# Kernel tuning notes

Measured on AMD Instinct MI355X. Metric: run time of the kernel, lower is better.

Reference implementation:

```python
import jax, jax.numpy as jnp
import numpy as np

N = 4096
CIN = 128
COUT = 128
J = 2
SLOPE = 0.2        # LeakyReLU negative slope (GAT-style)
NEG = -9.0e15      # mask fill value from the source
ATT = J * COUT     # att_slice


def _leaky(v):
    return jnp.where(v >= 0, v, SLOPE * v)


def setup_inputs() -> dict:
    key = jax.random.key(0)
    ks = jax.random.split(key, 12)
    x = jax.random.normal(ks[0], (N, CIN), dtype=jnp.float32)

    def sparse_op(k):
        kv, km = jax.random.split(k)
        vals = jax.random.normal(kv, (N, N), dtype=jnp.float32)
        mask = jax.random.uniform(km, (N, N)) < 0.05
        return jnp.where(mask, vals, 0.0)

    Lu = sparse_op(ks[1])
    Ld = sparse_op(ks[2])
    P = jax.random.normal(ks[3], (N, N), dtype=jnp.float32) * 0.01  # harmonic projector

    s = 1.0 / np.sqrt(CIN)
    Wi_w = jax.random.uniform(ks[4], (J, CIN, COUT), minval=-s, maxval=s)
    Wi_b = jax.random.uniform(ks[5], (J, COUT), minval=-s, maxval=s)
    Ws_w = jax.random.uniform(ks[6], (J, CIN, COUT), minval=-s, maxval=s)
    Ws_b = jax.random.uniform(ks[7], (J, COUT), minval=-s, maxval=s)
    Wh_w = jax.random.uniform(ks[8], (CIN, COUT), minval=-s, maxval=s)
    Wh_b = jax.random.uniform(ks[9], (COUT,), minval=-s, maxval=s)
    att_irr = jax.random.normal(ks[10], (2 * ATT, 1), dtype=jnp.float32) * 0.1
    att_sol = jax.random.normal(ks[11], (2 * ATT, 1), dtype=jnp.float32) * 0.1
    return {"x": x, "Lu": Lu, "Ld": Ld, "P": P,
            "Wi_w": Wi_w, "Wi_b": Wi_b, "Ws_w": Ws_w, "Ws_b": Ws_b,
            "Wh_w": Wh_w, "Wh_b": Wh_b, "att_irr": att_irr, "att_sol": att_sol}


def reference(x, Lu, Ld, P, Wi_w, Wi_b, Ws_w, Ws_b, Wh_w, Wh_b, att_irr, att_sol):
    n = x.shape[0]
    # concat_j W_irr[j](x) -> [N, J*COUT] (j-major matches torch.cat along dim=1)
    x_irr = (jnp.einsum('nc,jco->njo', x, Wi_w) + Wi_b[None]).reshape(n, ATT)
    x_sol = (jnp.einsum('nc,jco->njo', x, Ws_w) + Ws_b[None]).reshape(n, ATT)

    # GAT-style scores: E[i,j] = leaky(s1[i] + s2[j])
    E_irr = _leaky(x_irr @ att_irr[:ATT] + (x_irr @ att_irr[ATT:]).T)
    E_sol = _leaky(x_sol @ att_sol[:ATT] + (x_sol @ att_sol[ATT:]).T)
    E_irr = jnp.where(Ld != 0, E_irr, NEG)
    E_sol = jnp.where(Lu != 0, E_sol, NEG)
    alpha_irr = jax.nn.softmax(E_irr, axis=1)  # dropout: eval mode -> identity
    alpha_sol = jax.nn.softmax(E_sol, axis=1)

    z = (alpha_irr @ x) @ Wi_w[0] + Wi_b[0] + (alpha_sol @ x) @ Ws_w[0] + Ws_b[0]
    for p in range(1, J):  # Laplacian-power aggregation
        alpha_irr = alpha_irr @ Ld
        alpha_sol = alpha_sol @ Lu
        z = z + (alpha_irr @ x) @ Wi_w[p] + Wi_b[p]
        z = z + (alpha_sol @ x) @ Ws_w[p] + Ws_b[p]
    z = z + (P @ x) @ Wh_w + Wh_b
    return z
```

## Files before the change

kernel.cpp:

```cpp
#include <hip/hip_runtime.h>

#define NN 4096
#define IDX_CAP 512
#define SEG_CAP 160
#define SLOPE 0.2f

typedef float f4_t __attribute__((ext_vector_type(4)));
typedef __bf16 bf8v __attribute__((ext_vector_type(8)));
typedef float f32x16 __attribute__((ext_vector_type(16)));

#define V_OFF     0
#define C_OFF     512
#define BT_OFF    516
#define S_OFF     1024
#define HXI_OFF   32768
#define HXS_OFF   (HXI_OFF + NN*128)
#define UI_OFF    (HXS_OFF + NN*128)
#define US_OFF    (UI_OFF + NN*128)
#define XWH_OFF   (US_OFF + NN*128)
#define OI_OFF    (XWH_OFF + NN*128)
#define OS_OFF    (OI_OFF + NN*128)
#define ZP_OFF    (OS_OFF + NN*128)
#define WS_FLOATS (ZP_OFF + 8*NN*128)
#define IDX_BYTE_OFF ((size_t)WS_FLOATS * 4)
#define CNT_BYTE_OFF (IDX_BYTE_OFF + (size_t)2*NN*IDX_CAP*2)

#define XI(c)   ((c) + (((c) >> 5) << 2))

#define MAP_BR(bid)   (((bid) >> 2) & 1)
#define MAP_ROW(bid)  ((((bid) >> 3) << 2) | ((bid) & 3))

#define FRAG(c, k) ((size_t)((k) >> 4) * 2048 + (size_t)((c) >> 5) * 512 \
                    + (size_t)((((c) & 31) + 32 * (((k) >> 3) & 1)) * 8 + ((k) & 7)))

__device__ __forceinline__ unsigned short f2bf(float x) {
  unsigned u = __float_as_uint(x);
  return (unsigned short)((u + 0x7FFFu + ((u >> 16) & 1u)) >> 16);
}
__device__ __forceinline__ float bf2f(unsigned short h) {
  return __uint_as_float(((unsigned)h) << 16);
}
union BFU { unsigned short u[8]; bf8v v; };

__global__ __launch_bounds__(128) void k_prep(
    const float* __restrict__ Wi_w, const float* __restrict__ Wi_b,
    const float* __restrict__ Ws_w, const float* __restrict__ Ws_b,
    const float* __restrict__ Wh_b, const float* __restrict__ att_irr,
    const float* __restrict__ att_sol, float* __restrict__ ws) {
  const int t = threadIdx.x;
  float v1i = 0.f, v2i = 0.f, v1s = 0.f, v2s = 0.f;
  for (int j = 0; j < 2; ++j) {
    for (int o = 0; o < 128; ++o) {
      const float wi = Wi_w[j*16384 + t*128 + o];
      const float wv = Ws_w[j*16384 + t*128 + o];
      v1i += wi * att_irr[j*128 + o];
      v2i += wi * att_irr[256 + j*128 + o];
      v1s += wv * att_sol[j*128 + o];
      v2s += wv * att_sol[256 + j*128 + o];
    }
  }
  ws[V_OFF + t]       = v1i;
  ws[V_OFF + 128 + t] = v2i;
  ws[V_OFF + 256 + t] = v1s;
  ws[V_OFF + 384 + t] = v2s;
  ws[BT_OFF + t] = Wi_b[t] + Wi_b[128 + t] + Ws_b[t] + Ws_b[128 + t] + Wh_b[t];
  if (t < 4) {
    const float* bb = (t < 2) ? Wi_b : Ws_b;
    const float* aa = ((t < 2) ? att_irr : att_sol) + ((t & 1) ? 256 : 0);
    float c = 0.f;
    for (int k = 0; k < 256; ++k) c += bb[k] * aa[k];
    ws[C_OFF + t] = c;
  }
}

__global__ __launch_bounds__(256) void k_pre2(
    const float* __restrict__ x, const float* __restrict__ Wh_w,
    float* __restrict__ ws, unsigned short* __restrict__ xth,
    unsigned short* __restrict__ xtl) {
  __shared__ __align__(16) float At[32][33];
  __shared__ __align__(16) float Wt[32][144];
  const int t = threadIdx.x;

  if (blockIdx.x < 128) {
    const int rb = blockIdx.x;
    const int rg = t >> 4, cg = t & 15;
    const int r0 = rb * 32;
    float acc[2][8];
    #pragma unroll
    for (int i = 0; i < 2; ++i)
      #pragma unroll
      for (int j = 0; j < 8; ++j) acc[i][j] = 0.f;
    for (int k0 = 0; k0 < 128; k0 += 32) {
      __syncthreads();
      {
        const int row = t >> 3, kq = t & 7;
        const float4 av = *(const float4*)&x[(r0 + row)*128 + k0 + kq*4];
        At[row][kq*4+0] = av.x; At[row][kq*4+1] = av.y;
        At[row][kq*4+2] = av.z; At[row][kq*4+3] = av.w;
      }
      #pragma unroll
      for (int l = 0; l < 4; ++l) {
        const int idx = t + l*256;
        const int kr = idx >> 5, c4 = idx & 31;
        const float4 wv = *(const float4*)&Wh_w[(k0 + kr)*128 + c4*4];
        *(float4*)&Wt[kr][XI(c4*4)] = wv;
      }
      __syncthreads();
      #pragma unroll
      for (int k = 0; k < 32; ++k) {
        const float a0 = At[rg*2 + 0][k];
        const float a1 = At[rg*2 + 1][k];
        const float4 b0 = *(const float4*)&Wt[k][XI(cg*8)];
        const float4 b1 = *(const float4*)&Wt[k][XI(cg*8 + 4)];
        acc[0][0] += a0*b0.x; acc[0][1] += a0*b0.y; acc[0][2] += a0*b0.z; acc[0][3] += a0*b0.w;
        acc[0][4] += a0*b1.x; acc[0][5] += a0*b1.y; acc[0][6] += a0*b1.z; acc[0][7] += a0*b1.w;
        acc[1][0] += a1*b0.x; acc[1][1] += a1*b0.y; acc[1][2] += a1*b0.z; acc[1][3] += a1*b0.w;
        acc[1][4] += a1*b1.x; acc[1][5] += a1*b1.y; acc[1][6] += a1*b1.z; acc[1][7] += a1*b1.w;
      }
    }
    #pragma unroll
    for (int i = 0; i < 2; ++i) {
      const int r = r0 + rg*2 + i;
      #pragma unroll
      for (int j = 0; j < 8; ++j) {
        const int c = cg*8 + j;
        const float val = acc[i][j];
        const unsigned short h = f2bf(val);
        const unsigned short l = f2bf(val - bf2f(h));
        const size_t fa = FRAG(c, r);
        xth[fa] = h;
        xtl[fa] = l;
      }
    }
  } else {
    const int wave = t >> 6, lane = t & 63;
    const int row = (blockIdx.x - 128) * 4 + wave;
    const float* v = ws + V_OFF;
    const float x0 = x[row*128 + lane];
    const float x1 = x[row*128 + 64 + lane];
    float p0 = x0 * v[lane]       + x1 * v[64 + lane];
    float p1 = x0 * v[128 + lane] + x1 * v[192 + lane];
    float p2 = x0 * v[256 + lane] + x1 * v[320 + lane];
    float p3 = x0 * v[384 + lane] + x1 * v[448 + lane];
    #pragma unroll
    for (int off = 32; off; off >>= 1) {
      p0 += __shfl_down(p0, off);
      p1 += __shfl_down(p1, off);
      p2 += __shfl_down(p2, off);
      p3 += __shfl_down(p3, off);
    }
    if (lane == 0) {
      ws[S_OFF + row]          = p0 + ws[C_OFF + 0];
      ws[S_OFF + NN + row]     = p1 + ws[C_OFF + 1];
      ws[S_OFF + 2*NN + row]   = p2 + ws[C_OFF + 2];
      ws[S_OFF + 3*NN + row]   = p3 + ws[C_OFF + 3];
    }
  }
}

__global__ __launch_bounds__(256) void k_spmm_emit(
    const float* __restrict__ Ld, const float* __restrict__ Lu,
    const float* __restrict__ x, float* __restrict__ ws,
    unsigned short* __restrict__ idxbuf, int* __restrict__ cntbuf) {
  const int bid = blockIdx.x;
  const int br  = MAP_BR(bid);
  const int row = MAP_ROW(bid);
  const float* __restrict__ Lrow = (br ? Lu : Ld) + (size_t)row * NN;
  float* __restrict__ Hx = ws + (br ? HXS_OFF : HXI_OFF);
  unsigned short* __restrict__ idxg = idxbuf + (size_t)(br*NN + row) * IDX_CAP;
  const int t = threadIdx.x;
  const int w = t >> 6, lane = t & 63;
  const unsigned long long lmask = (1ull << lane) - 1ull;

  __shared__ short jseg[4][SEG_CAP];
  __shared__ float vseg[4][SEG_CAP];
  __shared__ int   wcnt[4];
  __shared__ int   off[5];
  __shared__ short jl[IDX_CAP];
  __shared__ float vl[IDX_CAP];
  __shared__ float red[4][128];

  const f4_t* __restrict__ Lrow4 = (const f4_t*)Lrow;
  f4_t lv[4];
  #pragma unroll
  for (int i = 0; i < 4; ++i) lv[i] = __builtin_nontemporal_load(&Lrow4[i*256 + t]);

  int base = 0;
  #pragma unroll
  for (int i = 0; i < 4; ++i) {
    #pragma unroll
    for (int c = 0; c < 4; ++c) {
      const float v = lv[i][c];
      const unsigned long long bm = __ballot(v != 0.f);
      if (v != 0.f) {
        const int pos = base + (int)__popcll(bm & lmask);
        if (pos < SEG_CAP) {
          jseg[w][pos] = (short)((i*256 + t)*4 + c);
          vseg[w][pos] = v;
        }
      }
      base += (int)__popcll(bm);
    }
  }
  if (lane == 0) wcnt[w] = base;
  __syncthreads();
  if (t == 0) {
    int o = 0, ov = 0;
    #pragma unroll
    for (int s = 0; s < 4; ++s) { off[s] = o; ov |= (wcnt[s] > SEG_CAP); o += wcnt[s]; }
    off[4] = (ov || o > IDX_CAP) ? (IDX_CAP + 1) : o;
    cntbuf[br*NN + row] = off[4];
  }
  __syncthreads();
  const int m = off[4];

  if (m <= IDX_CAP) {
    const int o = off[w], c = wcnt[w];
    for (int k = lane; k < c; k += 64) {
      const short j = jseg[w][k];
      jl[o + k] = j;
      vl[o + k] = vseg[w][k];
      idxg[o + k] = (unsigned short)j;
    }
  }
  __syncthreads();

  if (m <= IDX_CAP) {
    const f4_t* __restrict__ x4 = (const f4_t*)x;
    const int li = lane & 31, half = lane >> 5;
    f4_t acc = {0.f, 0.f, 0.f, 0.f};
    int p = w;
    for (; 2*(p + 12) + 1 < m; p += 16) {
      const int q0 = 2*p + half, q1 = 2*(p+4) + half,
                q2 = 2*(p+8) + half, q3 = 2*(p+12) + half;
      const int j0 = jl[q0], j1 = jl[q1], j2 = jl[q2], j3 = jl[q3];
      const float v0 = vl[q0], v1 = vl[q1], v2 = vl[q2], v3 = vl[q3];
      const f4_t g0 = x4[j0*32 + li];
      const f4_t g1 = x4[j1*32 + li];
      const f4_t g2 = x4[j2*32 + li];
      const f4_t g3 = x4[j3*32 + li];
      acc += v0*g0; acc += v1*g1; acc += v2*g2; acc += v3*g3;
    }
    for (; 2*p < m; p += 4) {
      const int q = 2*p + half;
      if (q < m) acc += vl[q] * x4[jl[q]*32 + li];
    }
    #pragma unroll
    for (int c = 0; c < 4; ++c) acc[c] += __shfl_xor(acc[c], 32);
    if (half == 0) {
      red[w][li*4+0] = acc[0]; red[w][li*4+1] = acc[1];
      red[w][li*4+2] = acc[2]; red[w][li*4+3] = acc[3];
    }
  } else {
    const float2* __restrict__ x2 = (const float2*)x;
    float acc0 = 0.f, acc1 = 0.f;
    for (int j = w*1024; j < (w+1)*1024; ++j) {
      const float v = Lrow[j];
      if (v != 0.f) {
        const float2 g = x2[j*64 + lane];
        acc0 += v*g.x; acc1 += v*g.y;
      }
    }
    red[w][lane*2]     = acc0;
    red[w][lane*2 + 1] = acc1;
  }
  __syncthreads();
  if (t < 128)
    Hx[row*128 + t] = red[0][t] + red[1][t] + red[2][t] + red[3][t];
}

__global__ __launch_bounds__(256) void k_ugemm(
    const float* __restrict__ x, const float* __restrict__ Wi_w,
    const float* __restrict__ Ws_w, float* __restrict__ ws) {
  const int rb = blockIdx.x;
  const int sel = blockIdx.y;
  const float* A[2]; const float* W[2]; float* out;
  if (sel == 0) { A[0]=x; W[0]=Wi_w; A[1]=ws+HXI_OFF; W[1]=Wi_w+16384; out=ws+UI_OFF; }
  else          { A[0]=x; W[0]=Ws_w; A[1]=ws+HXS_OFF; W[1]=Ws_w+16384; out=ws+US_OFF; }

  __shared__ __align__(16) float At[32][33];
  __shared__ __align__(16) float Wt[32][144];
  const int t = threadIdx.x;
  const int rg = t >> 4, cg = t & 15;
  const int r0 = rb * 32;
  float acc[2][8];
  #pragma unroll
  for (int i = 0; i < 2; ++i)
    #pragma unroll
    for (int j = 0; j < 8; ++j) acc[i][j] = 0.f;

  for (int ps = 0; ps < 2; ++ps) {
    const float* __restrict__ Ap = A[ps];
    const float* __restrict__ Wp = W[ps];
    for (int k0 = 0; k0 < 128; k0 += 32) {
      __syncthreads();
      {
        const int row = t >> 3, kq = t & 7;
        const float4 av = *(const float4*)&Ap[(r0 + row)*128 + k0 + kq*4];
        At[row][kq*4+0] = av.x; At[row][kq*4+1] = av.y;
        At[row][kq*4+2] = av.z; At[row][kq*4+3] = av.w;
      }
      #pragma unroll
      for (int l = 0; l < 4; ++l) {
        const int idx = t + l*256;
        const int kr = idx >> 5, c4 = idx & 31;
        const float4 wv = *(const float4*)&Wp[(k0 + kr)*128 + c4*4];
        *(float4*)&Wt[kr][XI(c4*4)] = wv;
      }
      __syncthreads();
      #pragma unroll
      for (int k = 0; k < 32; ++k) {
        const float a0 = At[rg*2 + 0][k];
        const float a1 = At[rg*2 + 1][k];
        const float4 b0 = *(const float4*)&Wt[k][XI(cg*8)];
        const float4 b1 = *(const float4*)&Wt[k][XI(cg*8 + 4)];
        acc[0][0] += a0*b0.x; acc[0][1] += a0*b0.y; acc[0][2] += a0*b0.z; acc[0][3] += a0*b0.w;
        acc[0][4] += a0*b1.x; acc[0][5] += a0*b1.y; acc[0][6] += a0*b1.z; acc[0][7] += a0*b1.w;
        acc[1][0] += a1*b0.x; acc[1][1] += a1*b0.y; acc[1][2] += a1*b0.z; acc[1][3] += a1*b0.w;
        acc[1][4] += a1*b1.x; acc[1][5] += a1*b1.y; acc[1][6] += a1*b1.z; acc[1][7] += a1*b1.w;
      }
    }
  }
  #pragma unroll
  for (int i = 0; i < 2; ++i) {
    const int r = r0 + rg*2 + i;
    #pragma unroll
    for (int j = 0; j < 8; ++j) out[r*128 + cg*8 + j] = acc[i][j];
  }
}

__global__ __launch_bounds__(256) void k_attn(
    const float* __restrict__ Ld, const float* __restrict__ Lu,
    float* __restrict__ ws, const unsigned short* __restrict__ idxbuf,
    const int* __restrict__ cntbuf) {
  const int bid = blockIdx.x;
  const int br  = MAP_BR(bid);
  const int row = MAP_ROW(bid);
  const float* __restrict__ U = ws + (br ? US_OFF : UI_OFF);
  float* __restrict__ O = ws + (br ? OS_OFF : OI_OFF);
  const float s1 = ws[S_OFF + (br ? 2*NN : 0) + row];
  const float* __restrict__ s2a = ws + S_OFF + (br ? 3*NN : NN);
  const int cnt = cntbuf[br*NN + row];
  const int t = threadIdx.x;
  const int w = t >> 6, lane = t & 63;

  __shared__ int   jl[IDX_CAP];
  __shared__ float el[IDX_CAP];
  __shared__ float red[4][128];
  __shared__ float rsum[256];
  __shared__ float dsh[4];

  if (cnt > 0 && cnt <= IDX_CAP) {
    const unsigned short* __restrict__ idx = idxbuf + (size_t)(br*NN + row) * IDX_CAP;
    float dpart = 0.f;
    for (int p = t; p < cnt; p += 256) {
      const int j = idx[p];
      const float sc = s1 + s2a[j];
      const float e = expf(sc >= 0.f ? sc : SLOPE * sc);
      jl[p] = j; el[p] = e; dpart += e;
    }
    rsum[t] = dpart;
    __syncthreads();
    if (t < 128) rsum[t] += rsum[t + 128];
    __syncthreads();
    if (t < 64) {
      float v = rsum[t] + rsum[t + 64];
      #pragma unroll
      for (int off = 32; off; off >>= 1) v += __shfl_down(v, off);
      if (t == 0) dsh[0] = v;
    }
    __syncthreads();
    const float den = dsh[0];
    const f4_t* __restrict__ U4 = (const f4_t*)U;
    const int li = lane & 31, half = lane >> 5;
    f4_t acc = {0.f, 0.f, 0.f, 0.f};
    int p = w;
    for (; 2*(p + 12) + 1 < cnt; p += 16) {
      const int q0 = 2*p + half, q1 = 2*(p+4) + half,
                q2 = 2*(p+8) + half, q3 = 2*(p+12) + half;
      const int j0 = jl[q0], j1 = jl[q1], j2 = jl[q2], j3 = jl[q3];
      const float e0 = el[q0], e1 = el[q1], e2 = el[q2], e3 = el[q3];
      const f4_t g0 = U4[j0*32 + li];
      const f4_t g1 = U4[j1*32 + li];
      const f4_t g2 = U4[j2*32 + li];
      const f4_t g3 = U4[j3*32 + li];
      acc += e0*g0; acc += e1*g1; acc += e2*g2; acc += e3*g3;
    }
    for (; 2*p < cnt; p += 4) {
      const int q = 2*p + half;
      if (q < cnt) acc += el[q] * U4[jl[q]*32 + li];
    }
    #pragma unroll
    for (int c = 0; c < 4; ++c) acc[c] += __shfl_xor(acc[c], 32);
    if (half == 0) {
      red[w][li*4+0] = acc[0]; red[w][li*4+1] = acc[1];
      red[w][li*4+2] = acc[2]; red[w][li*4+3] = acc[3];
    }
    __syncthreads();
    if (t < 128)
      O[row*128 + t] = (red[0][t] + red[1][t] + red[2][t] + red[3][t]) / den;
  } else if (cnt == 0) {
    const float2* __restrict__ U2 = (const float2*)U;
    float acc0 = 0.f, acc1 = 0.f;
    for (int j = w*1024; j < (w+1)*1024; ++j) {
      const float2 g = U2[j*64 + lane];
      acc0 += g.x; acc1 += g.y;
    }
    red[w][lane*2]     = acc0;
    red[w][lane*2 + 1] = acc1;
    __syncthreads();
    if (t < 128)
      O[row*128 + t] = (red[0][t] + red[1][t] + red[2][t] + red[3][t]) * (1.f / NN);
  } else {
    const float* __restrict__ Lrow = (br ? Lu : Ld) + (size_t)row * NN;
    const float2* __restrict__ U2 = (const float2*)U;
    float acc0 = 0.f, acc1 = 0.f, dp = 0.f;
    for (int j = w*1024; j < (w+1)*1024; ++j) {
      const float v = Lrow[j];
      if (v != 0.f) {
        const float sc = s1 + s2a[j];
        const float e = expf(sc >= 0.f ? sc : SLOPE * sc);
        const float2 g = U2[j*64 + lane];
        acc0 += e*g.x; acc1 += e*g.y;
        dp += e;
      }
    }
    if (lane == 0) dsh[w] = dp;
    red[w][lane*2]     = acc0;
    red[w][lane*2 + 1] = acc1;
    __syncthreads();
    const float den = dsh[0] + dsh[1] + dsh[2] + dsh[3];
    if (t < 128)
      O[row*128 + t] = (red[0][t] + red[1][t] + red[2][t] + red[3][t]) / den;
  }
}

__global__ __launch_bounds__(256) void k_pgemm(
    const float* __restrict__ P, const unsigned short* __restrict__ xth,
    const unsigned short* __restrict__ xtl, float* __restrict__ zpart) {
  const int t = threadIdx.x;
  const int w = t >> 6, lane = t & 63;
  const int la = lane & 31;
  const int koff = (lane >> 5) * 8;
  const int r0 = blockIdx.x * 32;
  const int kz = blockIdx.y;
  const int kb = kz * 512 + w * 128;

  f32x16 acc[4];
  #pragma unroll
  for (int n = 0; n < 4; ++n)
    #pragma unroll
    for (int e = 0; e < 16; ++e) acc[n][e] = 0.f;

  const float* __restrict__ arow = P + (size_t)(r0 + la) * NN + kb + koff;
  const unsigned short* __restrict__ bh_base = xth + (size_t)kb * 128 + lane * 8;
  const unsigned short* __restrict__ bl_base = xtl + (size_t)kb * 128 + lane * 8;

  f4_t a0 = __builtin_nontemporal_load((const f4_t*)arow);
  f4_t a1 = __builtin_nontemporal_load((const f4_t*)(arow + 4));
  for (int s = 0; s < 8; ++s) {
    f4_t na0 = a0, na1 = a1;
    if (s < 7) {
      na0 = __builtin_nontemporal_load((const f4_t*)(arow + (s + 1) * 16));
      na1 = __builtin_nontemporal_load((const f4_t*)(arow + (s + 1) * 16 + 4));
    }
    BFU ah, al;
    #pragma unroll
    for (int i = 0; i < 8; ++i) {
      const float f = (i < 4) ? a0[i] : a1[i - 4];
      const unsigned short h = f2bf(f);
      ah.u[i] = h;
      al.u[i] = f2bf(f - bf2f(h));
    }
    const unsigned short* __restrict__ bh_s = bh_base + s * 2048;
    const unsigned short* __restrict__ bl_s = bl_base + s * 2048;
    #pragma unroll
    for (int n = 0; n < 4; ++n) {
      const bf8v bh = *(const bf8v*)(bh_s + n * 512);
      const bf8v bl = *(const bf8v*)(bl_s + n * 512);
      acc[n] = __builtin_amdgcn_mfma_f32_32x32x16_bf16(ah.v, bh, acc[n], 0, 0, 0);
      acc[n] = __builtin_amdgcn_mfma_f32_32x32x16_bf16(al.v, bh, acc[n], 0, 0, 0);
      acc[n] = __builtin_amdgcn_mfma_f32_32x32x16_bf16(ah.v, bl, acc[n], 0, 0, 0);
    }
    a0 = na0; a1 = na1;
  }

  __shared__ float red[2][32][128];
  if (w < 2) {
    #pragma unroll
    for (int n = 0; n < 4; ++n)
      #pragma unroll
      for (int reg = 0; reg < 16; ++reg) {
        const int row = (reg & 3) + 8*(reg >> 2) + 4*(lane >> 5);
        red[w][row][32*n + la] = acc[n][reg];
      }
  }
  __syncthreads();
  if (w >= 2) {
    #pragma unroll
    for (int n = 0; n < 4; ++n)
      #pragma unroll
      for (int reg = 0; reg < 16; ++reg) {
        const int row = (reg & 3) + 8*(reg >> 2) + 4*(lane >> 5);
        red[w - 2][row][32*n + la] += acc[n][reg];
      }
  }
  __syncthreads();
  float* __restrict__ zp = zpart + (size_t)kz * NN * 128;
  #pragma unroll
  for (int i = 0; i < 8; ++i) {
    const int row = w * 8 + i;
    zp[(size_t)(r0 + row) * 128 + lane]      = red[0][row][lane]      + red[1][row][lane];
    zp[(size_t)(r0 + row) * 128 + 64 + lane] = red[0][row][64 + lane] + red[1][row][64 + lane];
  }
}

__global__ __launch_bounds__(256) void k_combine(const float* __restrict__ ws,
                                                 float* __restrict__ z) {
  const int i = blockIdx.x * 256 + threadIdx.x;
  const int col = i & 127;
  float acc = ws[BT_OFF + col] + ws[OI_OFF + i] + ws[OS_OFF + i];
  #pragma unroll
  for (int kz = 0; kz < 8; ++kz) acc += ws[ZP_OFF + kz*NN*128 + i];
  z[i] = acc;
}

extern "C" void kernel_launch(void* const* d_in, const int* in_sizes, int n_in,
                              void* d_out, int out_size, void* d_ws, size_t ws_size,
                              hipStream_t stream) {
  const float* x       = (const float*)d_in[0];
  const float* Lu      = (const float*)d_in[1];
  const float* Ld      = (const float*)d_in[2];
  const float* P       = (const float*)d_in[3];
  const float* Wi_w    = (const float*)d_in[4];
  const float* Wi_b    = (const float*)d_in[5];
  const float* Ws_w    = (const float*)d_in[6];
  const float* Ws_b    = (const float*)d_in[7];
  const float* Wh_w    = (const float*)d_in[8];
  const float* Wh_b    = (const float*)d_in[9];
  const float* att_irr = (const float*)d_in[10];
  const float* att_sol = (const float*)d_in[11];
  float* z  = (float*)d_out;
  float* ws = (float*)d_ws;
  unsigned short* idxbuf = (unsigned short*)((char*)d_ws + IDX_BYTE_OFF);
  int*            cntbuf = (int*)((char*)d_ws + CNT_BYTE_OFF);
  float*          zpart  = ws + ZP_OFF;
  unsigned short* xth    = (unsigned short*)(ws + XWH_OFF);
  unsigned short* xtl    = xth + (size_t)128 * NN;

  k_prep<<<1, 128, 0, stream>>>(Wi_w, Wi_b, Ws_w, Ws_b, Wh_b, att_irr, att_sol, ws);
  k_pre2<<<1152, 256, 0, stream>>>(x, Wh_w, ws, xth, xtl);
  k_spmm_emit<<<2 * NN, 256, 0, stream>>>(Ld, Lu, x, ws, idxbuf, cntbuf);
  {
    dim3 g(128, 2);
    k_ugemm<<<g, 256, 0, stream>>>(x, Wi_w, Ws_w, ws);
  }
  k_attn<<<2 * NN, 256, 0, stream>>>(Ld, Lu, ws, idxbuf, cntbuf);
  {
    dim3 g(128, 8);
    k_pgemm<<<g, 256, 0, stream>>>(P, xth, xtl, zpart);
  }
  k_combine<<<NN * 128 / 256, 256, 0, stream>>>(ws, z);
}
```

Measured before the change: 353.8 us.

## Map one row per wavefront in sparse emit and attention kernels

```diff
diff --git a/kernel.cpp b/kernel.cpp
--- a/kernel.cpp
+++ b/kernel.cpp
@@ -2,7 +2,6 @@
 
 #define NN 4096
 #define IDX_CAP 512
-#define SEG_CAP 160
 #define SLOPE 0.2f
 
 typedef float f4_t __attribute__((ext_vector_type(4)));
@@ -27,8 +26,8 @@
 
 #define XI(c)   ((c) + (((c) >> 5) << 2))
 
-#define MAP_BR(bid)   (((bid) >> 2) & 1)
-#define MAP_ROW(bid)  ((((bid) >> 3) << 2) | ((bid) & 3))
+#define BMAP_BR(bid)    (((bid) >> 2) & 1)
+#define BMAP_RBLK(bid)  ((((bid) >> 3) << 2) | ((bid) & 3))
 
 #define FRAG(c, k) ((size_t)((k) >> 4) * 2048 + (size_t)((c) >> 5) * 512 \
                     + (size_t)((((c) & 31) + 32 * (((k) >> 3) & 1)) * 8 + ((k) & 7)))
@@ -163,110 +162,85 @@
     const float* __restrict__ x, float* __restrict__ ws,
     unsigned short* __restrict__ idxbuf, int* __restrict__ cntbuf) {
   const int bid = blockIdx.x;
-  const int br  = MAP_BR(bid);
-  const int row = MAP_ROW(bid);
+  const int br  = BMAP_BR(bid);
+  const int w = threadIdx.x >> 6, lane = threadIdx.x & 63;
+  const int row = BMAP_RBLK(bid) * 4 + w;
   const float* __restrict__ Lrow = (br ? Lu : Ld) + (size_t)row * NN;
   float* __restrict__ Hx = ws + (br ? HXS_OFF : HXI_OFF);
   unsigned short* __restrict__ idxg = idxbuf + (size_t)(br*NN + row) * IDX_CAP;
-  const int t = threadIdx.x;
-  const int w = t >> 6, lane = t & 63;
   const unsigned long long lmask = (1ull << lane) - 1ull;
 
-  __shared__ short jseg[4][SEG_CAP];
-  __shared__ float vseg[4][SEG_CAP];
-  __shared__ int   wcnt[4];
-  __shared__ int   off[5];
-  __shared__ short jl[IDX_CAP];
-  __shared__ float vl[IDX_CAP];
-  __shared__ float red[4][128];
+  __shared__ short jl[4][IDX_CAP];
+  __shared__ float vl[4][IDX_CAP];
 
   const f4_t* __restrict__ Lrow4 = (const f4_t*)Lrow;
-  f4_t lv[4];
-  #pragma unroll
-  for (int i = 0; i < 4; ++i) lv[i] = __builtin_nontemporal_load(&Lrow4[i*256 + t]);
-
   int base = 0;
   #pragma unroll
-  for (int i = 0; i < 4; ++i) {
-    #pragma unroll
-    for (int c = 0; c < 4; ++c) {
-      const float v = lv[i][c];
-      const unsigned long long bm = __ballot(v != 0.f);
-      if (v != 0.f) {
-        const int pos = base + (int)__popcll(bm & lmask);
-        if (pos < SEG_CAP) {
-          jseg[w][pos] = (short)((i*256 + t)*4 + c);
-          vseg[w][pos] = v;
+  for (int c = 0; c < 4; ++c) {
+    f4_t lv[4];
+    #pragma unroll
+    for (int i = 0; i < 4; ++i)
+      lv[i] = __builtin_nontemporal_load(&Lrow4[c*256 + i*64 + lane]);
+    #pragma unroll
+    for (int i = 0; i < 4; ++i) {
+      #pragma unroll
+      for (int cc = 0; cc < 4; ++cc) {
+        const float v = lv[i][cc];
+        const unsigned long long bm = __ballot(v != 0.f);
+        if (v != 0.f) {
+          const int pos = base + (int)__popcll(bm & lmask);
+          if (pos < IDX_CAP) {
+            jl[w][pos] = (short)((c*256 + i*64 + lane)*4 + cc);
+            vl[w][pos] = v;
+          }
         }
-      }
-      base += (int)__popcll(bm);
-    }
-  }
-  if (lane == 0) wcnt[w] = base;
-  __syncthreads();
-  if (t == 0) {
-    int o = 0, ov = 0;
-    #pragma unroll
-    for (int s = 0; s < 4; ++s) { off[s] = o; ov |= (wcnt[s] > SEG_CAP); o += wcnt[s]; }
-    off[4] = (ov || o > IDX_CAP) ? (IDX_CAP + 1) : o;
-    cntbuf[br*NN + row] = off[4];
-  }
-  __syncthreads();
-  const int m = off[4];
+        base += (int)__popcll(bm);
+      }
+    }
+  }
+  const int m = base;
+  if (lane == 0) cntbuf[br*NN + row] = m;
 
   if (m <= IDX_CAP) {
-    const int o = off[w], c = wcnt[w];
-    for (int k = lane; k < c; k += 64) {
-      const short j = jseg[w][k];
-      jl[o + k] = j;
-      vl[o + k] = vseg[w][k];
-      idxg[o + k] = (unsigned short)j;
-    }
-  }
-  __syncthreads();
-
-  if (m <= IDX_CAP) {
+    for (int p = lane; p < m; p += 64) idxg[p] = (unsigned short)jl[w][p];
+
     const f4_t* __restrict__ x4 = (const f4_t*)x;
     const int li = lane & 31, half = lane >> 5;
     f4_t acc = {0.f, 0.f, 0.f, 0.f};
-    int p = w;
-    for (; 2*(p + 12) + 1 < m; p += 16) {
-      const int q0 = 2*p + half, q1 = 2*(p+4) + half,
-                q2 = 2*(p+8) + half, q3 = 2*(p+12) + half;
-      const int j0 = jl[q0], j1 = jl[q1], j2 = jl[q2], j3 = jl[q3];
-      const float v0 = vl[q0], v1 = vl[q1], v2 = vl[q2], v3 = vl[q3];
-      const f4_t g0 = x4[j0*32 + li];
-      const f4_t g1 = x4[j1*32 + li];
-      const f4_t g2 = x4[j2*32 + li];
-      const f4_t g3 = x4[j3*32 + li];
-      acc += v0*g0; acc += v1*g1; acc += v2*g2; acc += v3*g3;
-    }
-    for (; 2*p < m; p += 4) {
+    int p = 0;
+    for (; 2*(p + 3) + 1 < m; p += 4) {
+      int jj[4]; float vv[4];
+      #pragma unroll
+      for (int u = 0; u < 4; ++u) {
+        const int q = 2*(p + u) + half;
+        jj[u] = jl[w][q]; vv[u] = vl[w][q];
+      }
+      f4_t gg[4];
+      #pragma unroll
+      for (int u = 0; u < 4; ++u) gg[u] = x4[jj[u]*32 + li];
+      #pragma unroll
+      for (int u = 0; u < 4; ++u) acc += vv[u] * gg[u];
+    }
+    for (; 2*p < m; ++p) {
       const int q = 2*p + half;
-      if (q < m) acc += vl[q] * x4[jl[q]*32 + li];
+      if (q < m) acc += vl[w][q] * x4[jl[w][q]*32 + li];
     }
     #pragma unroll
     for (int c = 0; c < 4; ++c) acc[c] += __shfl_xor(acc[c], 32);
-    if (half == 0) {
-      red[w][li*4+0] = acc[0]; red[w][li*4+1] = acc[1];
-      red[w][li*4+2] = acc[2]; red[w][li*4+3] = acc[3];
-    }
+    if (half == 0) *(f4_t*)&Hx[row*128 + li*4] = acc;
   } else {
     const float2* __restrict__ x2 = (const float2*)x;
     float acc0 = 0.f, acc1 = 0.f;
-    for (int j = w*1024; j < (w+1)*1024; ++j) {
+    for (int j = 0; j < NN; ++j) {
       const float v = Lrow[j];
       if (v != 0.f) {
         const float2 g = x2[j*64 + lane];
         acc0 += v*g.x; acc1 += v*g.y;
       }
     }
-    red[w][lane*2]     = acc0;
-    red[w][lane*2 + 1] = acc1;
-  }
-  __syncthreads();
-  if (t < 128)
-    Hx[row*128 + t] = red[0][t] + red[1][t] + red[2][t] + red[3][t];
+    Hx[row*128 + lane*2]     = acc0;
+    Hx[row*128 + lane*2 + 1] = acc1;
+  }
 }
 
 __global__ __launch_bounds__(256) void k_ugemm(
@@ -334,88 +308,72 @@
     float* __restrict__ ws, const unsigned short* __restrict__ idxbuf,
     const int* __restrict__ cntbuf) {
   const int bid = blockIdx.x;
-  const int br  = MAP_BR(bid);
-  const int row = MAP_ROW(bid);
+  const int br  = BMAP_BR(bid);
+  const int w = threadIdx.x >> 6, lane = threadIdx.x & 63;
+  const int row = BMAP_RBLK(bid) * 4 + w;
   const float* __restrict__ U = ws + (br ? US_OFF : UI_OFF);
   float* __restrict__ O = ws + (br ? OS_OFF : OI_OFF);
   const float s1 = ws[S_OFF + (br ? 2*NN : 0) + row];
   const float* __restrict__ s2a = ws + S_OFF + (br ? 3*NN : NN);
   const int cnt = cntbuf[br*NN + row];
-  const int t = threadIdx.x;
-  const int w = t >> 6, lane = t & 63;
-
-  __shared__ int   jl[IDX_CAP];
-  __shared__ float el[IDX_CAP];
-  __shared__ float red[4][128];
-  __shared__ float rsum[256];
-  __shared__ float dsh[4];
+
+  __shared__ short jl[4][IDX_CAP];
+  __shared__ float el[4][IDX_CAP];
 
   if (cnt > 0 && cnt <= IDX_CAP) {
     const unsigned short* __restrict__ idx = idxbuf + (size_t)(br*NN + row) * IDX_CAP;
     float dpart = 0.f;
-    for (int p = t; p < cnt; p += 256) {
+    for (int p = lane; p < cnt; p += 64) {
       const int j = idx[p];
       const float sc = s1 + s2a[j];
       const float e = expf(sc >= 0.f ? sc : SLOPE * sc);
-      jl[p] = j; el[p] = e; dpart += e;
-    }
-    rsum[t] = dpart;
-    __syncthreads();
-    if (t < 128) rsum[t] += rsum[t + 128];
-    __syncthreads();
-    if (t < 64) {
-      float v = rsum[t] + rsum[t + 64];
-      #pragma unroll
-      for (int off = 32; off; off >>= 1) v += __shfl_down(v, off);
-      if (t == 0) dsh[0] = v;
-    }
-    __syncthreads();
-    const float den = dsh[0];
+      jl[w][p] = (short)j; el[w][p] = e; dpart += e;
+    }
+    #pragma unroll
+    for (int off = 32; off; off >>= 1) dpart += __shfl_xor(dpart, off);
+    const float rden = 1.f / dpart;
+
     const f4_t* __restrict__ U4 = (const f4_t*)U;
     const int li = lane & 31, half = lane >> 5;
     f4_t acc = {0.f, 0.f, 0.f, 0.f};
-    int p = w;
-    for (; 2*(p + 12) + 1 < cnt; p += 16) {
-      const int q0 = 2*p + half, q1 = 2*(p+4) + half,
-                q2 = 2*(p+8) + half, q3 = 2*(p+12) + half;
-      const int j0 = jl[q0], j1 = jl[q1], j2 = jl[q2], j3 = jl[q3];
-      const float e0 = el[q0], e1 = el[q1], e2 = el[q2], e3 = el[q3];
-      const f4_t g0 = U4[j0*32 + li];
-      const f4_t g1 = U4[j1*32 + li];
-      const f4_t g2 = U4[j2*32 + li];
-      const f4_t g3 = U4[j3*32 + li];
-      acc += e0*g0; acc += e1*g1; acc += e2*g2; acc += e3*g3;
-    }
-    for (; 2*p < cnt; p += 4) {
+    int p = 0;
+    for (; 2*(p + 3) + 1 < cnt; p += 4) {
+      int jj[4]; float ee[4];
+      #pragma unroll
+      for (int u = 0; u < 4; ++u) {
+        const int q = 2*(p + u) + half;
+        jj[u] = jl[w][q]; ee[u] = el[w][q];
+      }
+      f4_t gg[4];
+      #pragma unroll
+      for (int u = 0; u < 4; ++u) gg[u] = U4[jj[u]*32 + li];
+      #pragma unroll
+      for (int u = 0; u < 4; ++u) acc += ee[u] * gg[u];
+    }
+    for (; 2*p < cnt; ++p) {
       const int q = 2*p + half;
-      if (q < cnt) acc += el[q] * U4[jl[q]*32 + li];
+      if (q < cnt) acc += el[w][q] * U4[jl[w][q]*32 + li];
     }
     #pragma unroll
     for (int c = 0; c < 4; ++c) acc[c] += __shfl_xor(acc[c], 32);
     if (half == 0) {
-      red[w][li*4+0] = acc[0]; red[w][li*4+1] = acc[1];
-      red[w][li*4+2] = acc[2]; red[w][li*4+3] = acc[3];
-    }
-    __syncthreads();
-    if (t < 128)
-      O[row*128 + t] = (red[0][t] + red[1][t] + red[2][t] + red[3][t]) / den;
+      acc *= rden;
+      *(f4_t*)&O[row*128 + li*4] = acc;
+    }
   } else if (cnt == 0) {
     const float2* __restrict__ U2 = (const float2*)U;
     float acc0 = 0.f, acc1 = 0.f;
-    for (int j = w*1024; j < (w+1)*1024; ++j) {
+    for (int j = 0; j < NN; ++j) {
       const float2 g = U2[j*64 + lane];
       acc0 += g.x; acc1 += g.y;
     }
-    red[w][lane*2]     = acc0;
-    red[w][lane*2 + 1] = acc1;
-    __syncthreads();
-    if (t < 128)
-      O[row*128 + t] = (red[0][t] + red[1][t] + red[2][t] + red[3][t]) * (1.f / NN);
+    O[row*128 + lane*2]     = acc0 * (1.f / NN);
+    O[row*128 + lane*2 + 1] = acc1 * (1.f / NN);
   } else {
     const float* __restrict__ Lrow = (br ? Lu : Ld) + (size_t)row * NN;
     const float2* __restrict__ U2 = (const float2*)U;
     float acc0 = 0.f, acc1 = 0.f, dp = 0.f;
-    for (int j = w*1024; j < (w+1)*1024; ++j) {
+    for (int j = 0; j < NN; ++j) {
       const float v = Lrow[j];
       if (v != 0.f) {
         const float sc = s1 + s2a[j];
@@ -425,13 +383,8 @@
         dp += e;
       }
     }
-    if (lane == 0) dsh[w] = dp;
-    red[w][lane*2]     = acc0;
-    red[w][lane*2 + 1] = acc1;
-    __syncthreads();
-    const float den = dsh[0] + dsh[1] + dsh[2] + dsh[3];
-    if (t < 128)
-      O[row*128 + t] = (red[0][t] + red[1][t] + red[2][t] + red[3][t]) / den;
+    O[row*128 + lane*2]     = acc0 / dp;
+    O[row*128 + lane*2 + 1] = acc1 / dp;
   }
 }
 
@@ -550,12 +503,12 @@
 
   k_prep<<<1, 128, 0, stream>>>(Wi_w, Wi_b, Ws_w, Ws_b, Wh_b, att_irr, att_sol, ws);
   k_pre2<<<1152, 256, 0, stream>>>(x, Wh_w, ws, xth, xtl);
-  k_spmm_emit<<<2 * NN, 256, 0, stream>>>(Ld, Lu, x, ws, idxbuf, cntbuf);
+  k_spmm_emit<<<2 * NN / 4, 256, 0, stream>>>(Ld, Lu, x, ws, idxbuf, cntbuf);
   {
     dim3 g(128, 2);
     k_ugemm<<<g, 256, 0, stream>>>(x, Wi_w, Ws_w, ws);
   }
-  k_attn<<<2 * NN, 256, 0, stream>>>(Ld, Lu, ws, idxbuf, cntbuf);
+  k_attn<<<2 * NN / 4, 256, 0, stream>>>(Ld, Lu, ws, idxbuf, cntbuf);
   {
     dim3 g(128, 8);
     k_pgemm<<<g, 256, 0, stream>>>(P, xth, xtl, zpart);
```

Result: no change. 354.7 us (+0.3%).
